# Kernel tuning notes

Measured on AMD Instinct MI355X. Metric: run time of the kernel, lower is better.

## Reference

```python
import jax, jax.numpy as jnp
import numpy as np

B, S, D, E, TOP_K = 4, 4096, 2048, 64, 2


def setup_inputs() -> dict:
    key = jax.random.key(0)
    kx, kw, kb = jax.random.split(key, 3)
    x = jax.random.normal(kx, (B, S, D), dtype=jnp.float32)
    # nn.Linear(d_model, n_expert): weight (E, D), bias (E,)
    bound = 1.0 / np.sqrt(D)
    W = jax.random.uniform(kw, (E, D), dtype=jnp.float32, minval=-bound, maxval=bound)
    b = jax.random.uniform(kb, (E,), dtype=jnp.float32, minval=-bound, maxval=bound)
    return {"x": x, "W": W, "b": b}


def reference(x, W, b):
    # logits: (B, S, E)
    logits = jnp.einsum("bsd,ed->bse", x, W) + b
    top_k_logits, ids = jax.lax.top_k(logits, TOP_K)  # (B,S,K) each
    # scatter top-k logits into a -inf filled tensor along the expert dim
    n = B * S
    flat = jnp.full((n, E), -jnp.inf, dtype=logits.dtype)
    rows = jnp.arange(n)[:, None]  # (n,1)
    flat = flat.at[rows, ids.reshape(n, TOP_K)].set(top_k_logits.reshape(n, TOP_K))
    sparse_logits = flat.reshape(B, S, E)
    router_output = jax.nn.softmax(sparse_logits, axis=-1)  # zeros outside top-k
    return router_output, ids
```

## Files before the change

### kernel.cpp

```cpp
#include <hip/hip_runtime.h>
#include <math.h>

#define NTOK 16384
#define D_   2048
#define E_   64
#define TPB  32
#define NKC  (D_/32)
#define NS   16

typedef _Float16 f16x8 __attribute__((ext_vector_type(8)));
typedef float    f32x4 __attribute__((ext_vector_type(4)));

#define LSCALE      256.0f
#define LSCALE2_INV (1.0f/65536.0f)

#define LOG_STRIDE  65
#define RES_OFF_F   (TPB*LOG_STRIDE)
#define SMEM_FLOATS 16384

__global__ __launch_bounds__(256)
void prep_w(const float* __restrict__ W,
            _Float16* __restrict__ wh, _Float16* __restrict__ wl)
{
    const int idx = blockIdx.x * 256 + threadIdx.x;
    const int l  = idx & 63;
    const int kc = (idx >> 6) & 63;
    const int nt = idx >> 12;
    const int e  = nt * 16 + (l & 15);
    const int g  = l >> 4;
    const float* src = W + (size_t)e * D_ + kc * 32 + g * 4;
    const float4 f0 = *reinterpret_cast<const float4*>(src);
    const float4 f1 = *reinterpret_cast<const float4*>(src + 16);
    const float v[8] = {f0.x, f0.y, f0.z, f0.w, f1.x, f1.y, f1.z, f1.w};
    f16x8 h, lo;
#pragma unroll
    for (int j = 0; j < 8; ++j) {
        const float vs = v[j] * LSCALE;
        const _Float16 hj = (_Float16)vs;
        h[j]  = hj;
        lo[j] = (_Float16)(vs - (float)hj);
    }
    *reinterpret_cast<f16x8*>(wh + (size_t)idx * 8) = h;
    *reinterpret_cast<f16x8*>(wl + (size_t)idx * 8) = lo;
}

__device__ __forceinline__ void stage16(const void* g, void* l) {
    __builtin_amdgcn_global_load_lds(
        (const __attribute__((address_space(1))) void*)g,
        (__attribute__((address_space(3))) void*)l, 16, 0, 0);
}

__global__ __launch_bounds__(512, 4)
void router_mfma(const float* __restrict__ x,
                 const _Float16* __restrict__ wh,
                 const _Float16* __restrict__ wl,
                 const float* __restrict__ bias,
                 float* __restrict__ out)
{
    __shared__ float smem[SMEM_FLOATS];
    char* sb = (char*)smem;

    const int tid = threadIdx.x;
    const int l   = tid & 63;
    const int w   = __builtin_amdgcn_readfirstlane(tid >> 6);
    const int mt  = w >> 2;
    const int nt  = w & 3;
    const int T0  = blockIdx.x * TPB;
    const int g   = l >> 4;

    f32x4 acc = {0.f, 0.f, 0.f, 0.f};

    const int c1   = 512 + tid;
    const int row0 = (tid >> 3) & 31, slot0 = (tid & 7) ^ (row0 & 7);
    const int row1 = (c1  >> 3) & 31, slot1 = (c1  & 7) ^ (row1 & 7);
    const float* xs0 = x + (size_t)(T0 + row0) * D_ + (tid >> 8) * 32 + slot0 * 4;
    const float* xs1 = x + (size_t)(T0 + row1) * D_ + (c1  >> 8) * 32 + slot1 * 4;

    auto STAGE_X = [&](int sup) {
        const int bo = (sup & 3) << 14;
        stage16(xs0 + (size_t)sup * 128, sb + bo + (w << 10));
        stage16(xs1 + (size_t)sup * 128, sb + bo + 8192 + (w << 10));
    };

    const _Float16* bh_base = wh + ((size_t)nt * NKC * 64 + l) * 8;
    const _Float16* bl_base = wl + ((size_t)nt * NKC * 64 + l) * 8;
    auto LDB_H = [&](int kc) { return *reinterpret_cast<const f16x8*>(bh_base + (size_t)kc * 512); };
    auto LDB_L = [&](int kc) { return *reinterpret_cast<const f16x8*>(bl_base + (size_t)kc * 512); };

    const int arow   = mt * 16 + (l & 15);
    const int r7_    = arow & 7;
    const int xa_off = arow * 128 + ((g       ^ r7_) << 4);
    const int xb_off = arow * 128 + (((4 + g) ^ r7_) << 4);

    auto COMPUTE = [&](int pb, f16x8 bh, f16x8 bl) {
        const float4 xa = *reinterpret_cast<const float4*>(sb + pb + xa_off);
        const float4 xb = *reinterpret_cast<const float4*>(sb + pb + xb_off);
        f16x8 ah, al_;
        {
            float vs;
            vs = xa.x * LSCALE; ah[0] = (_Float16)vs; al_[0] = (_Float16)(vs - (float)ah[0]);
            vs = xa.y * LSCALE; ah[1] = (_Float16)vs; al_[1] = (_Float16)(vs - (float)ah[1]);
            vs = xa.z * LSCALE; ah[2] = (_Float16)vs; al_[2] = (_Float16)(vs - (float)ah[2]);
            vs = xa.w * LSCALE; ah[3] = (_Float16)vs; al_[3] = (_Float16)(vs - (float)ah[3]);
            vs = xb.x * LSCALE; ah[4] = (_Float16)vs; al_[4] = (_Float16)(vs - (float)ah[4]);
            vs = xb.y * LSCALE; ah[5] = (_Float16)vs; al_[5] = (_Float16)(vs - (float)ah[5]);
            vs = xb.z * LSCALE; ah[6] = (_Float16)vs; al_[6] = (_Float16)(vs - (float)ah[6]);
            vs = xb.w * LSCALE; ah[7] = (_Float16)vs; al_[7] = (_Float16)(vs - (float)ah[7]);
        }
        acc = __builtin_amdgcn_mfma_f32_16x16x32_f16(ah,  bh, acc, 0, 0, 0);
        acc = __builtin_amdgcn_mfma_f32_16x16x32_f16(al_, bh, acc, 0, 0, 0);
        acc = __builtin_amdgcn_mfma_f32_16x16x32_f16(ah,  bl, acc, 0, 0, 0);
    };

    f16x8 bhc[4], blc[4], bhn[4], bln[4];
#pragma unroll
    for (int j = 0; j < 4; ++j) { bhc[j] = LDB_H(j); blc[j] = LDB_L(j); }
    STAGE_X(0); STAGE_X(1); STAGE_X(2);
    asm volatile("s_waitcnt vmcnt(4)" ::: "memory");
    __builtin_amdgcn_s_barrier();

    for (int s = 0; s < NS; ++s) {
        const int K  = s << 2;
        const int bo = (s & 3) << 14;
        if (s < NS - 1) {
#pragma unroll
            for (int j = 0; j < 4; ++j) { bhn[j] = LDB_H(K + 4 + j); bln[j] = LDB_L(K + 4 + j); }
        }
        COMPUTE(bo,         bhc[0], blc[0]);
        COMPUTE(bo | 4096,  bhc[1], blc[1]);
        COMPUTE(bo | 8192,  bhc[2], blc[2]);
        COMPUTE(bo | 12288, bhc[3], blc[3]);
        if (s + 3 < NS) STAGE_X(s + 3);
        if (s < NS - 1) {
#pragma unroll
            for (int j = 0; j < 4; ++j) { bhc[j] = bhn[j]; blc[j] = bln[j]; }
            asm volatile("s_waitcnt vmcnt(10)" ::: "memory");
            __builtin_amdgcn_s_barrier();
        }
    }

    {
        float* logits = smem;
        const int rr0 = mt * 16 + g * 4;
        const int cc  = nt * 16 + (l & 15);
#pragma unroll
        for (int r = 0; r < 4; ++r)
            logits[(rr0 + r) * LOG_STRIDE + cc] = acc[r] * LSCALE2_INV;
    }
    __syncthreads();

    float* res = smem + RES_OFF_F;
    if (tid < TPB) {
        const float* lg = smem + tid * LOG_STRIDE;
        float m1 = -INFINITY, m2 = -INFINITY;
        int i1 = 0, i2 = 0;
        for (int e = 0; e < E_; ++e) {
            const float v = lg[e] + bias[e];
            if (v > m1)      { m2 = m1; i2 = i1; m1 = v; i1 = e; }
            else if (v > m2) { m2 = v;  i2 = e; }
        }
        const float ex  = expf(m2 - m1);
        const float den = 1.f + ex;
        res[tid*4+0] = 1.f / den;
        res[tid*4+1] = ex / den;
        res[tid*4+2] = (float)i1;
        res[tid*4+3] = (float)i2;
    }
    __syncthreads();

    const size_t obase = (size_t)T0 * E_;
#pragma unroll
    for (int i = 0; i < (TPB * E_) / 512; ++i) {
        const int f = i * 512 + tid;
        const int t = f >> 6;
        const int e = f & 63;
        const float p1 = res[t*4+0];
        const float p2 = res[t*4+1];
        const int   i1 = (int)res[t*4+2];
        const int   i2 = (int)res[t*4+3];
        float v = 0.f;
        if (e == i1)      v = p1;
        else if (e == i2) v = p2;
        out[obase + f] = v;
    }
    if (tid < TPB * 2) {
        out[(size_t)NTOK * E_ + (size_t)T0 * 2 + tid] =
            res[(tid >> 1) * 4 + 2 + (tid & 1)];
    }
}

extern "C" void kernel_launch(void* const* d_in, const int* in_sizes, int n_in,
                              void* d_out, int out_size, void* d_ws, size_t ws_size,
                              hipStream_t stream) {
    const float* x = (const float*)d_in[0];
    const float* W = (const float*)d_in[1];
    const float* b = (const float*)d_in[2];
    float* out     = (float*)d_out;
    _Float16* wh   = (_Float16*)d_ws;
    _Float16* wl   = wh + (size_t)4 * NKC * 64 * 8;

    hipLaunchKernelGGL(prep_w, dim3(64), dim3(256), 0, stream, W, wh, wl);
    hipLaunchKernelGGL(router_mfma, dim3(NTOK / TPB), dim3(512), 0, stream,
                       x, wh, wl, b, out);
}
```

Measured before the change: 59.74 us.

## Shrink router tile to 16 tokens per 4-wave block with deeper x staging ring

Cuts each block from 32 tokens and 8 waves to 16 tokens and 4 waves, one wave per 16-expert column tile. The x staging is reorganised into a 16-slot ring of 2 KB pages, each holding one 32-wide k-chunk, with a two-superstep prefetch distance and explicit vmcnt waits plus sched barriers. This doubles the block count and halves LDS per block, aiming for more blocks in flight and better latency hiding. The cost is that each block now reloads the full W fragments for half as many tokens, doubling W traffic per token.

```diff
diff --git a/kernel.cpp b/kernel.cpp
--- a/kernel.cpp
+++ b/kernel.cpp
@@ -4,7 +4,7 @@
 #define NTOK 16384
 #define D_   2048
 #define E_   64
-#define TPB  32
+#define TPB  16
 #define NKC  (D_/32)
 #define NS   16
 
@@ -14,9 +14,7 @@
 #define LSCALE      256.0f
 #define LSCALE2_INV (1.0f/65536.0f)
 
-#define LOG_STRIDE  65
-#define RES_OFF_F   (TPB*LOG_STRIDE)
-#define SMEM_FLOATS 16384
+#define SMEM_FLOATS 8192
 
 __global__ __launch_bounds__(256)
 void prep_w(const float* __restrict__ W,
@@ -50,7 +48,7 @@
         (__attribute__((address_space(3))) void*)l, 16, 0, 0);
 }
 
-__global__ __launch_bounds__(512, 4)
+__global__ __launch_bounds__(256, 4)
 void router_mfma(const float* __restrict__ x,
                  const _Float16* __restrict__ wh,
                  const _Float16* __restrict__ wl,
@@ -63,95 +61,104 @@
     const int tid = threadIdx.x;
     const int l   = tid & 63;
     const int w   = __builtin_amdgcn_readfirstlane(tid >> 6);
-    const int mt  = w >> 2;
-    const int nt  = w & 3;
     const int T0  = blockIdx.x * TPB;
     const int g   = l >> 4;
 
     f32x4 acc = {0.f, 0.f, 0.f, 0.f};
 
-    const int c1   = 512 + tid;
-    const int row0 = (tid >> 3) & 31, slot0 = (tid & 7) ^ (row0 & 7);
-    const int row1 = (c1  >> 3) & 31, slot1 = (c1  & 7) ^ (row1 & 7);
-    const float* xs0 = x + (size_t)(T0 + row0) * D_ + (tid >> 8) * 32 + slot0 * 4;
-    const float* xs1 = x + (size_t)(T0 + row1) * D_ + (c1  >> 8) * 32 + slot1 * 4;
-
-    auto STAGE_X = [&](int sup) {
-        const int bo = (sup & 3) << 14;
-        stage16(xs0 + (size_t)sup * 128, sb + bo + (w << 10));
-        stage16(xs1 + (size_t)sup * 128, sb + bo + 8192 + (w << 10));
+    const int srow = l >> 3;
+    const int ssl  = (l & 7) ^ (srow & 7);
+    const float* xsA = x + (size_t)(T0 + srow) * D_ + ssl * 4;
+    const float* xsB = xsA + (size_t)8 * D_;
+
+    auto STAGE = [&](int kcs) {
+        char* pg = sb + ((kcs & 15) << 11);
+        stage16(xsA + (size_t)kcs * 32, pg);
+        stage16(xsB + (size_t)kcs * 32, pg + 1024);
     };
 
-    const _Float16* bh_base = wh + ((size_t)nt * NKC * 64 + l) * 8;
-    const _Float16* bl_base = wl + ((size_t)nt * NKC * 64 + l) * 8;
-    auto LDB_H = [&](int kc) { return *reinterpret_cast<const f16x8*>(bh_base + (size_t)kc * 512); };
-    auto LDB_L = [&](int kc) { return *reinterpret_cast<const f16x8*>(bl_base + (size_t)kc * 512); };
-
-    const int arow   = mt * 16 + (l & 15);
+    const _Float16* bh_base = wh + ((size_t)w * NKC * 64 + l) * 8;
+    const _Float16* bl_base = wl + ((size_t)w * NKC * 64 + l) * 8;
+
+    const int arow   = l & 15;
     const int r7_    = arow & 7;
     const int xa_off = arow * 128 + ((g       ^ r7_) << 4);
     const int xb_off = arow * 128 + (((4 + g) ^ r7_) << 4);
 
-    auto COMPUTE = [&](int pb, f16x8 bh, f16x8 bl) {
-        const float4 xa = *reinterpret_cast<const float4*>(sb + pb + xa_off);
-        const float4 xb = *reinterpret_cast<const float4*>(sb + pb + xb_off);
-        f16x8 ah, al_;
-        {
-            float vs;
-            vs = xa.x * LSCALE; ah[0] = (_Float16)vs; al_[0] = (_Float16)(vs - (float)ah[0]);
-            vs = xa.y * LSCALE; ah[1] = (_Float16)vs; al_[1] = (_Float16)(vs - (float)ah[1]);
-            vs = xa.z * LSCALE; ah[2] = (_Float16)vs; al_[2] = (_Float16)(vs - (float)ah[2]);
-            vs = xa.w * LSCALE; ah[3] = (_Float16)vs; al_[3] = (_Float16)(vs - (float)ah[3]);
-            vs = xb.x * LSCALE; ah[4] = (_Float16)vs; al_[4] = (_Float16)(vs - (float)ah[4]);
-            vs = xb.y * LSCALE; ah[5] = (_Float16)vs; al_[5] = (_Float16)(vs - (float)ah[5]);
-            vs = xb.z * LSCALE; ah[6] = (_Float16)vs; al_[6] = (_Float16)(vs - (float)ah[6]);
-            vs = xb.w * LSCALE; ah[7] = (_Float16)vs; al_[7] = (_Float16)(vs - (float)ah[7]);
-        }
-        acc = __builtin_amdgcn_mfma_f32_16x16x32_f16(ah,  bh, acc, 0, 0, 0);
-        acc = __builtin_amdgcn_mfma_f32_16x16x32_f16(al_, bh, acc, 0, 0, 0);
-        acc = __builtin_amdgcn_mfma_f32_16x16x32_f16(ah,  bl, acc, 0, 0, 0);
-    };
-
-    f16x8 bhc[4], blc[4], bhn[4], bln[4];
-#pragma unroll
-    for (int j = 0; j < 4; ++j) { bhc[j] = LDB_H(j); blc[j] = LDB_L(j); }
-    STAGE_X(0); STAGE_X(1); STAGE_X(2);
+    f16x8 BhC[4], BlC[4], BhN[4], BlN[4];
+
+#pragma unroll
+    for (int j = 0; j < 4; ++j) {
+        BhC[j] = *reinterpret_cast<const f16x8*>(bh_base + (size_t)j * 512);
+        BlC[j] = *reinterpret_cast<const f16x8*>(bl_base + (size_t)j * 512);
+    }
+    STAGE(w); STAGE(4 + w);
     asm volatile("s_waitcnt vmcnt(4)" ::: "memory");
+    __builtin_amdgcn_sched_barrier(0);
     __builtin_amdgcn_s_barrier();
 
     for (int s = 0; s < NS; ++s) {
-        const int K  = s << 2;
-        const int bo = (s & 3) << 14;
+        const int K = s << 2;
         if (s < NS - 1) {
 #pragma unroll
-            for (int j = 0; j < 4; ++j) { bhn[j] = LDB_H(K + 4 + j); bln[j] = LDB_L(K + 4 + j); }
-        }
-        COMPUTE(bo,         bhc[0], blc[0]);
-        COMPUTE(bo | 4096,  bhc[1], blc[1]);
-        COMPUTE(bo | 8192,  bhc[2], blc[2]);
-        COMPUTE(bo | 12288, bhc[3], blc[3]);
-        if (s + 3 < NS) STAGE_X(s + 3);
-        if (s < NS - 1) {
-#pragma unroll
-            for (int j = 0; j < 4; ++j) { bhc[j] = bhn[j]; blc[j] = bln[j]; }
+            for (int j = 0; j < 4; ++j) {
+                BhN[j] = *reinterpret_cast<const f16x8*>(bh_base + (size_t)(K + 4 + j) * 512);
+                BlN[j] = *reinterpret_cast<const f16x8*>(bl_base + (size_t)(K + 4 + j) * 512);
+            }
+        }
+        if (s < NS - 2) STAGE(((s + 2) << 2) + w);
+        if (s < NS - 2)      { asm volatile("s_waitcnt vmcnt(12)" ::: "memory"); }
+        else if (s == NS - 2){ asm volatile("s_waitcnt vmcnt(10)" ::: "memory"); }
+        else                 { asm volatile("s_waitcnt vmcnt(0)"  ::: "memory"); }
+        __builtin_amdgcn_sched_barrier(0);
+
+#pragma unroll
+        for (int j = 0; j < 4; ++j) {
+            const int kc = K + j;
+            const char* pg = sb + ((kc & 15) << 11);
+            const float4 xa = *reinterpret_cast<const float4*>(pg + xa_off);
+            const float4 xb = *reinterpret_cast<const float4*>(pg + xb_off);
+            f16x8 ah, al_;
+            {
+                float vs;
+                vs = xa.x * LSCALE; ah[0] = (_Float16)vs; al_[0] = (_Float16)(vs - (float)ah[0]);
+                vs = xa.y * LSCALE; ah[1] = (_Float16)vs; al_[1] = (_Float16)(vs - (float)ah[1]);
+                vs = xa.z * LSCALE; ah[2] = (_Float16)vs; al_[2] = (_Float16)(vs - (float)ah[2]);
+                vs = xa.w * LSCALE; ah[3] = (_Float16)vs; al_[3] = (_Float16)(vs - (float)ah[3]);
+                vs = xb.x * LSCALE; ah[4] = (_Float16)vs; al_[4] = (_Float16)(vs - (float)ah[4]);
+                vs = xb.y * LSCALE; ah[5] = (_Float16)vs; al_[5] = (_Float16)(vs - (float)ah[5]);
+                vs = xb.z * LSCALE; ah[6] = (_Float16)vs; al_[6] = (_Float16)(vs - (float)ah[6]);
+                vs = xb.w * LSCALE; ah[7] = (_Float16)vs; al_[7] = (_Float16)(vs - (float)ah[7]);
+            }
+            acc = __builtin_amdgcn_mfma_f32_16x16x32_f16(ah,  BhC[j], acc, 0, 0, 0);
+            acc = __builtin_amdgcn_mfma_f32_16x16x32_f16(al_, BhC[j], acc, 0, 0, 0);
+            acc = __builtin_amdgcn_mfma_f32_16x16x32_f16(ah,  BlC[j], acc, 0, 0, 0);
+        }
+#pragma unroll
+        for (int j = 0; j < 4; ++j) { BhC[j] = BhN[j]; BlC[j] = BlN[j]; }
+
+        if (s < NS - 2) {
             asm volatile("s_waitcnt vmcnt(10)" ::: "memory");
             __builtin_amdgcn_s_barrier();
+        } else if (s == NS - 2) {
+            asm volatile("s_waitcnt vmcnt(8)" ::: "memory");
+            __builtin_amdgcn_s_barrier();
         }
     }
 
     {
         float* logits = smem;
-        const int rr0 = mt * 16 + g * 4;
-        const int cc  = nt * 16 + (l & 15);
+        const int rr0 = g * 4;
+        const int cc  = w * 16 + (l & 15);
 #pragma unroll
         for (int r = 0; r < 4; ++r)
-            logits[(rr0 + r) * LOG_STRIDE + cc] = acc[r] * LSCALE2_INV;
+            logits[(rr0 + r) * 65 + cc] = acc[r] * LSCALE2_INV;
     }
     __syncthreads();
 
-    float* res = smem + RES_OFF_F;
+    float* res = smem + TPB * 65;
     if (tid < TPB) {
-        const float* lg = smem + tid * LOG_STRIDE;
+        const float* lg = smem + tid * 65;
         float m1 = -INFINITY, m2 = -INFINITY;
         int i1 = 0, i2 = 0;
         for (int e = 0; e < E_; ++e) {
@@ -170,8 +177,8 @@
 
     const size_t obase = (size_t)T0 * E_;
 #pragma unroll
-    for (int i = 0; i < (TPB * E_) / 512; ++i) {
-        const int f = i * 512 + tid;
+    for (int i = 0; i < (TPB * E_) / 256; ++i) {
+        const int f = i * 256 + tid;
         const int t = f >> 6;
         const int e = f & 63;
         const float p1 = res[t*4+0];
@@ -200,6 +207,6 @@
     _Float16* wl   = wh + (size_t)4 * NKC * 64 * 8;
 
     hipLaunchKernelGGL(prep_w, dim3(64), dim3(256), 0, stream, W, wh, wl);
-    hipLaunchKernelGGL(router_mfma, dim3(NTOK / TPB), dim3(512), 0, stream,
+    hipLaunchKernelGGL(router_mfma, dim3(NTOK / TPB), dim3(256), 0, stream,
                        x, wh, wl, b, out);
 }
```

Measured after the change: 55.40 us. 1.08x faster.
